# Optimization experiments

Hardware: AMD Instinct MI355X
Metric: run time of the kernel (lower is better)

## Reference

```python
import jax, jax.numpy as jnp
import numpy as np

N_NODES = 100000
N_EDGES = 1600000
D = 64
BN_EPS = 1e-5


def setup_inputs() -> dict:
    key = jax.random.key(0)
    ks = jax.random.split(key, 10)
    s = 1.0 / np.sqrt(D)
    return {
        "features": jax.random.normal(ks[0], (N_NODES, D), dtype=jnp.float32),
        "src": jax.random.randint(ks[1], (N_EDGES,), 0, N_NODES, dtype=jnp.int32),
        "dst": jax.random.randint(ks[2], (N_EDGES,), 0, N_NODES, dtype=jnp.int32),
        "eps": jnp.zeros((), dtype=jnp.float32),
        "W1": jax.random.uniform(ks[3], (D, D), jnp.float32, -s, s),
        "b1": jax.random.uniform(ks[4], (D,), jnp.float32, -s, s),
        "W2": jax.random.uniform(ks[5], (D, D), jnp.float32, -s, s),
        "b2": jax.random.uniform(ks[6], (D,), jnp.float32, -s, s),
        "gamma": jnp.ones((D,), dtype=jnp.float32),
        "beta": jnp.zeros((D,), dtype=jnp.float32),
    }


def reference(features, src, dst, eps, W1, b1, W2, b2, gamma, beta):
    h_in = features
    # message passing: gather src node features, scatter-sum to dst (fn.copy_u + fn.sum)
    neigh = jax.ops.segment_sum(features[src], dst, num_segments=N_NODES)  # [N, D]
    # eps-weighted self term
    h = (1.0 + eps) * features + neigh
    # apply_func MLP: Linear -> ReLU -> Linear
    h = jnp.maximum(h @ W1 + b1, 0.0) @ W2 + b2
    # BatchNorm1d over nodes (training-mode batch statistics)
    mean = jnp.mean(h, axis=0)
    var = jnp.var(h, axis=0)
    h = (h - mean) * jax.lax.rsqrt(var + BN_EPS) * gamma + beta
    # activation
    h = jnp.maximum(h, 0.0)
    # residual (indim == outdim)
    h = h_in + h
    # dropout p=0 -> identity
    return h
```

## Files before the change

kernel.cpp:

```cpp
#include <hip/hip_runtime.h>
#include <hip/hip_fp16.h>

#define N_NODES 100000
#define N_EDGES 1600000
#define D 64
#define BN_EPS 1e-5f
#define NSHARD 64

#define NBKT 256
#define NPB 391
#define BKT_CAP 13056
#define NBBLK 391
#define SORT_T 1024

typedef _Float16 half8 __attribute__((ext_vector_type(8)));
typedef float f32x4 __attribute__((ext_vector_type(4)));

__global__ __launch_bounds__(256) void prep_k(
    const int* __restrict__ src, const int* __restrict__ dst,
    int* __restrict__ bkt_cnt, int* __restrict__ bktbuf,
    const float* __restrict__ feat, __half* __restrict__ feat16,
    const float* __restrict__ W1, const float* __restrict__ W2,
    _Float16* __restrict__ w1t, _Float16* __restrict__ w2t)
{
    __shared__ int h[NBKT], base[NBKT], cur[NBKT];
    const int blk = blockIdx.x;
    const int t = threadIdx.x;

    if (blk < NBBLK) {
        h[t] = 0; cur[t] = 0;
        __syncthreads();
        const int e0 = blk * 4096;
        int pk[16], b[16];
        #pragma unroll
        for (int i = 0; i < 16; ++i) {
            int e = e0 + i * 256 + t;
            if (e < N_EDGES) {
                int d = dst[e];
                b[i] = d / NPB;
                pk[i] = (src[e] << 9) | (d - b[i] * NPB);
                atomicAdd(&h[b[i]], 1);
            } else {
                b[i] = -1;
            }
        }
        __syncthreads();
        base[t] = atomicAdd(&bkt_cnt[t], h[t]);
        __syncthreads();
        #pragma unroll
        for (int i = 0; i < 16; ++i) {
            if (b[i] >= 0) {
                int p = atomicAdd(&cur[b[i]], 1);
                bktbuf[(size_t)b[i] * BKT_CAP + base[b[i]] + p] = pk[i];
            }
        }
    } else if (blk < NBBLK + 3125) {
        size_t i = ((size_t)(blk - NBBLK) * 256 + t) * 8;
        if (i < (size_t)N_NODES * D) {
            float4 v0 = *(const float4*)(feat + i);
            float4 v1 = *(const float4*)(feat + i + 4);
            __half2 o[4];
            o[0] = __floats2half2_rn(v0.x, v0.y);
            o[1] = __floats2half2_rn(v0.z, v0.w);
            o[2] = __floats2half2_rn(v1.x, v1.y);
            o[3] = __floats2half2_rn(v1.z, v1.w);
            *(float4*)(feat16 + i) = *(float4*)o;
        }
    } else {
        const int n = t >> 2;
        const int k0 = (t & 3) * 16;
        _Float16 o1[16], o2[16];
        #pragma unroll
        for (int j = 0; j < 16; ++j) {
            o1[j] = (_Float16)W1[(k0 + j) * 64 + n];
            o2[j] = (_Float16)W2[(k0 + j) * 64 + n];
        }
        #pragma unroll
        for (int j = 0; j < 16; j += 8) {
            *(half8*)(w1t + n * 64 + k0 + j) = *(half8*)&o1[j];
            *(half8*)(w2t + n * 64 + k0 + j) = *(half8*)&o2[j];
        }
    }
}

__global__ __launch_bounds__(SORT_T) void sortp_k(
    const int* __restrict__ bktbuf, const int* __restrict__ bkt_cnt,
    int* __restrict__ rowptr, int* __restrict__ col)
{
    __shared__ int h[NPB];
    __shared__ int cur[NPB];
    __shared__ int part[SORT_T];
    __shared__ int bsc[NBKT];

    const int b = blockIdx.x;
    const int t = threadIdx.x;
    const int nb0 = b * NPB;
    const int nodes_in = min(NPB, N_NODES - nb0);
    const int cnt = bkt_cnt[b];
    const int* buf = bktbuf + (size_t)b * BKT_CAP;

    if (t < NBKT) bsc[t] = bkt_cnt[t];
    __syncthreads();
    for (int off = 1; off < NBKT; off <<= 1) {
        int x = 0;
        if (t < NBKT) {
            x = bsc[t];
            if (t >= off) x += bsc[t - off];
        }
        __syncthreads();
        if (t < NBKT) bsc[t] = x;
        __syncthreads();
    }
    const int gbase = bsc[b] - cnt;

    if (t < NPB) h[t] = 0;
    __syncthreads();

    for (int i = t; i < cnt; i += SORT_T)
        atomicAdd(&h[buf[i] & 511], 1);
    __syncthreads();

    int a = (t < NPB) ? h[t] : 0;
    part[t] = a;
    __syncthreads();
    for (int off = 1; off < SORT_T; off <<= 1) {
        int x = part[t];
        int u = (t >= off) ? part[t - off] : 0;
        __syncthreads();
        part[t] = x + u;
        __syncthreads();
    }
    int excl = part[t] - a;
    if (t < NPB) {
        cur[t] = excl;
        if (t < nodes_in) rowptr[nb0 + t] = gbase + excl;
    }
    if (b == NBKT - 1 && t == 0) rowptr[N_NODES] = N_EDGES;
    __syncthreads();

    for (int i = t; i < cnt; i += SORT_T) {
        int pk = buf[i];
        int slot = atomicAdd(&cur[pk & 511], 1);
        col[gbase + slot] = pk >> 9;
    }
}

__device__ __forceinline__ void acc16(float* a, float4 r0, float4 r1)
{
    const __half2* h0 = (const __half2*)&r0;
    const __half2* h1 = (const __half2*)&r1;
    #pragma unroll
    for (int i = 0; i < 4; ++i) {
        float2 f = __half22float2(h0[i]);
        a[2 * i]     += f.x;
        a[2 * i + 1] += f.y;
    }
    #pragma unroll
    for (int i = 0; i < 4; ++i) {
        float2 f = __half22float2(h1[i]);
        a[8 + 2 * i]     += f.x;
        a[8 + 2 * i + 1] += f.y;
    }
}

__global__ __launch_bounds__(256) void gatherq_k(
    const __half* __restrict__ feat16, const int* __restrict__ rowptr,
    const int* __restrict__ col, const float* __restrict__ epsp,
    __half* __restrict__ x16)
{
    const int t = threadIdx.x;
    const int node = blockIdx.x * 64 + (t >> 2);
    if (node >= N_NODES) return;
    const int c = (t & 3) << 4;

    const int lo = rowptr[node];
    const int hi = rowptr[node + 1];

    float a[16];
    #pragma unroll
    for (int i = 0; i < 16; ++i) a[i] = 0.f;

    int e = lo;
    for (; e + 3 < hi; e += 4) {
        const int s0 = col[e], s1 = col[e + 1], s2 = col[e + 2], s3 = col[e + 3];
        const __half* p0 = feat16 + (size_t)s0 * 64 + c;
        const __half* p1 = feat16 + (size_t)s1 * 64 + c;
        const __half* p2 = feat16 + (size_t)s2 * 64 + c;
        const __half* p3 = feat16 + (size_t)s3 * 64 + c;
        float4 r00 = *(const float4*)(p0), r01 = *(const float4*)(p0 + 8);
        float4 r10 = *(const float4*)(p1), r11 = *(const float4*)(p1 + 8);
        float4 r20 = *(const float4*)(p2), r21 = *(const float4*)(p2 + 8);
        float4 r30 = *(const float4*)(p3), r31 = *(const float4*)(p3 + 8);
        acc16(a, r00, r01);
        acc16(a, r10, r11);
        acc16(a, r20, r21);
        acc16(a, r30, r31);
    }
    for (; e < hi; ++e) {
        const __half* p = feat16 + (size_t)col[e] * 64 + c;
        float4 r0 = *(const float4*)(p), r1 = *(const float4*)(p + 8);
        acc16(a, r0, r1);
    }

    const float epsv = 1.0f + epsp[0];
    const size_t gb = (size_t)node * 64 + c;
    float4 s0 = *(const float4*)(feat16 + gb);
    float4 s1 = *(const float4*)(feat16 + gb + 8);
    const __half2* h0 = (const __half2*)&s0;
    const __half2* h1 = (const __half2*)&s1;
    __half2 o[8];
    #pragma unroll
    for (int i = 0; i < 4; ++i) {
        float2 f = __half22float2(h0[i]);
        o[i] = __floats2half2_rn(fmaf(epsv, f.x, a[2 * i]),
                                 fmaf(epsv, f.y, a[2 * i + 1]));
    }
    #pragma unroll
    for (int i = 0; i < 4; ++i) {
        float2 f = __half22float2(h1[i]);
        o[4 + i] = __floats2half2_rn(fmaf(epsv, f.x, a[8 + 2 * i]),
                                     fmaf(epsv, f.y, a[8 + 2 * i + 1]));
    }
    *(float4*)(x16 + gb)     = *(float4*)&o[0];
    *(float4*)(x16 + gb + 8) = *(float4*)&o[4];
}

__global__ __launch_bounds__(256) void mfma_mlp2_k(
    const __half* __restrict__ x16,
    const _Float16* __restrict__ w1t, const _Float16* __restrict__ w2t,
    const float* __restrict__ b1, const float* __restrict__ b2,
    __half* __restrict__ h216, float* __restrict__ stats)
{
    __shared__ __align__(16) _Float16 xts[64 * 72];

    const int t    = threadIdx.x;
    const int w    = t >> 6;
    const int lane = t & 63;
    const int m    = lane & 15;
    const int q    = lane >> 4;
    const int rbase = w * 16;
    const int nb   = blockIdx.x * 64;

    const _Float16* xg = (const _Float16*)x16 + (size_t)(nb + rbase + m) * 64 + q * 8;
    half8 a0 = *(const half8*)(xg);
    half8 a1 = *(const half8*)(xg + 32);

    f32x4 acc[4];
    #pragma unroll
    for (int jt = 0; jt < 4; ++jt) {
        const float bias = b1[jt * 16 + m];
        acc[jt] = (f32x4){bias, bias, bias, bias};
        const _Float16* bw = w1t + (jt * 16 + m) * 64 + q * 8;
        half8 bf0 = *(const half8*)(bw);
        half8 bf1 = *(const half8*)(bw + 32);
        acc[jt] = __builtin_amdgcn_mfma_f32_16x16x32_f16(a0, bf0, acc[jt], 0, 0, 0);
        acc[jt] = __builtin_amdgcn_mfma_f32_16x16x32_f16(a1, bf1, acc[jt], 0, 0, 0);
    }

    #pragma unroll
    for (int jt = 0; jt < 4; ++jt)
        #pragma unroll
        for (int r = 0; r < 4; ++r)
            xts[(rbase + q * 4 + r) * 72 + jt * 16 + m] =
                (_Float16)fmaxf(acc[jt][r], 0.0f);
    asm volatile("s_waitcnt lgkmcnt(0)" ::: "memory");

    const _Float16* xw = &xts[(rbase + m) * 72 + q * 8];
    half8 c0 = *(const half8*)(xw);
    half8 c1 = *(const half8*)(xw + 32);

    f32x4 acc2[4];
    #pragma unroll
    for (int jt = 0; jt < 4; ++jt) {
        const float bias = b2[jt * 16 + m];
        acc2[jt] = (f32x4){bias, bias, bias, bias};
        const _Float16* bw = w2t + (jt * 16 + m) * 64 + q * 8;
        half8 bf0 = *(const half8*)(bw);
        half8 bf1 = *(const half8*)(bw + 32);
        acc2[jt] = __builtin_amdgcn_mfma_f32_16x16x32_f16(c0, bf0, acc2[jt], 0, 0, 0);
        acc2[jt] = __builtin_amdgcn_mfma_f32_16x16x32_f16(c1, bf1, acc2[jt], 0, 0, 0);
    }
    asm volatile("s_waitcnt lgkmcnt(0)" ::: "memory");

    float psums[4], psqs[4];
    #pragma unroll
    for (int jt = 0; jt < 4; ++jt) {
        float ps = 0.f, pq = 0.f;
        #pragma unroll
        for (int r = 0; r < 4; ++r) {
            const int row = rbase + q * 4 + r;
            const float v = acc2[jt][r];
            const float vv = (nb + row < N_NODES) ? v : 0.f;
            ps += vv;
            pq += vv * vv;
            xts[row * 72 + jt * 16 + m] = (_Float16)v;
        }
        ps += __shfl_xor(ps, 16, 64); ps += __shfl_xor(ps, 32, 64);
        pq += __shfl_xor(pq, 16, 64); pq += __shfl_xor(pq, 32, 64);
        psums[jt] = ps; psqs[jt] = pq;
    }
    if (lane < 16) {
        float* sp = stats + (size_t)(blockIdx.x & (NSHARD - 1)) * 128;
        #pragma unroll
        for (int jt = 0; jt < 4; ++jt) {
            unsafeAtomicAdd(sp + jt * 16 + lane,      psums[jt]);
            unsafeAtomicAdd(sp + 64 + jt * 16 + lane, psqs[jt]);
        }
    }
    asm volatile("s_waitcnt lgkmcnt(0)" ::: "memory");

    {
        const int rr = lane >> 2;
        const int cc = (lane & 3) * 16;
        const int gn = nb + rbase + rr;
        if (gn < N_NODES) {
            float4 r0 = *(const float4*)&xts[(rbase + rr) * 72 + cc];
            float4 r1 = *(const float4*)&xts[(rbase + rr) * 72 + cc + 8];
            *(float4*)(h216 + (size_t)gn * 64 + cc)     = r0;
            *(float4*)(h216 + (size_t)gn * 64 + cc + 8) = r1;
        }
    }
}

__global__ void bnstats_k(const float* __restrict__ stats,
                          const float* __restrict__ gamma,
                          const float* __restrict__ beta,
                          float* __restrict__ sf)
{
    int j = threadIdx.x;
    float s = 0.f, q = 0.f;
    for (int c = 0; c < NSHARD; ++c) {
        s += stats[c * 128 + j];
        q += stats[c * 128 + 64 + j];
    }
    const float invN = 1.0f / (float)N_NODES;
    float mean  = s * invN;
    float var   = q * invN - mean * mean;
    float scale = gamma[j] * rsqrtf(var + BN_EPS);
    sf[j]      = scale;
    sf[64 + j] = beta[j] - mean * scale;
}

__global__ __launch_bounds__(256) void finish16_k(
    const float* __restrict__ feat, const __half* __restrict__ h216,
    const float* __restrict__ sf, float* __restrict__ out)
{
    __shared__ float scs[64], shs[64];
    if (threadIdx.x < 64) {
        scs[threadIdx.x] = sf[threadIdx.x];
        shs[threadIdx.x] = sf[64 + threadIdx.x];
    }
    __syncthreads();
    size_t i = (size_t)blockIdx.x * 256 + threadIdx.x;
    if (i < (size_t)N_NODES * D / 4) {
        int j = (int)((i * 4) & 63);
        const __half2* hp = (const __half2*)(h216 + i * 4);
        float2 h0 = __half22float2(hp[0]);
        float2 h1 = __half22float2(hp[1]);
        float4 f = *(const float4*)(feat + i * 4);
        float4 o;
        o.x = fmaxf(fmaf(h0.x, scs[j + 0], shs[j + 0]), 0.f) + f.x;
        o.y = fmaxf(fmaf(h0.y, scs[j + 1], shs[j + 1]), 0.f) + f.y;
        o.z = fmaxf(fmaf(h1.x, scs[j + 2], shs[j + 2]), 0.f) + f.z;
        o.w = fmaxf(fmaf(h1.y, scs[j + 3], shs[j + 3]), 0.f) + f.w;
        *(float4*)(out + i * 4) = o;
    }
}

#define OCAP 7680

__global__ __launch_bounds__(256) void bucket2_k(
    const int* __restrict__ src, const int* __restrict__ dst,
    int* __restrict__ bkt_cnt, int2* __restrict__ bktbuf)
{
    __shared__ int h[NBKT], base[NBKT], cur[NBKT];
    const int t = threadIdx.x;
    h[t] = 0; cur[t] = 0;
    __syncthreads();
    const int e0 = blockIdx.x * 4096;
    int s[16], d[16], b[16];
    #pragma unroll
    for (int i = 0; i < 16; ++i) {
        int e = e0 + i * 256 + t;
        if (e < N_EDGES) {
            s[i] = src[e];
            d[i] = dst[e];
            b[i] = d[i] / NPB;
            atomicAdd(&h[b[i]], 1);
        } else {
            b[i] = -1;
        }
    }
    __syncthreads();
    base[t] = atomicAdd(&bkt_cnt[t], h[t]);
    __syncthreads();
    #pragma unroll
    for (int i = 0; i < 16; ++i) {
        if (b[i] >= 0) {
            int p = atomicAdd(&cur[b[i]], 1);
            bktbuf[(size_t)b[i] * OCAP + base[b[i]] + p] = make_int2(s[i], d[i]);
        }
    }
}

__global__ __launch_bounds__(SORT_T) void sort2_k(
    const int2* __restrict__ bktbuf, const int* __restrict__ bkt_cnt,
    int* __restrict__ rowptr, int* __restrict__ col)
{
    __shared__ int h[NPB];
    __shared__ int cur[NPB];
    __shared__ int part[SORT_T];
    __shared__ int bsc[NBKT];

    const int b = blockIdx.x;
    const int t = threadIdx.x;
    const int nb0 = b * NPB;
    const int nodes_in = min(NPB, N_NODES - nb0);
    const int cnt = bkt_cnt[b];
    const int2* buf = bktbuf + (size_t)b * OCAP;

    if (t < NBKT) bsc[t] = bkt_cnt[t];
    __syncthreads();
    for (int off = 1; off < NBKT; off <<= 1) {
        int x = 0;
        if (t < NBKT) {
            x = bsc[t];
            if (t >= off) x += bsc[t - off];
        }
        __syncthreads();
        if (t < NBKT) bsc[t] = x;
        __syncthreads();
    }
    const int gbase = bsc[b] - cnt;

    if (t < NPB) h[t] = 0;
    __syncthreads();

    for (int i = t; i < cnt; i += SORT_T)
        atomicAdd(&h[buf[i].y - nb0], 1);
    __syncthreads();

    int a = (t < NPB) ? h[t] : 0;
    part[t] = a;
    __syncthreads();
    for (int off = 1; off < SORT_T; off <<= 1) {
        int x = part[t];
        int u = (t >= off) ? part[t - off] : 0;
        __syncthreads();
        part[t] = x + u;
        __syncthreads();
    }
    int excl = part[t] - a;
    if (t < NPB) {
        cur[t] = excl;
        if (t < nodes_in) rowptr[nb0 + t] = gbase + excl;
    }
    if (b == NBKT - 1 && t == 0) rowptr[N_NODES] = N_EDGES;
    __syncthreads();

    for (int i = t; i < cnt; i += SORT_T) {
        int2 r = buf[i];
        int slot = atomicAdd(&cur[r.y - nb0], 1);
        col[gbase + slot] = r.x;
    }
}

__global__ __launch_bounds__(256) void gather32_k(
    const float* __restrict__ feat, const int* __restrict__ rowptr,
    const int* __restrict__ col, const float* __restrict__ epsp,
    float* __restrict__ x)
{
    int node = blockIdx.x * 4 + (threadIdx.x >> 6);
    int lane = threadIdx.x & 63;
    if (node >= N_NODES) return;
    int g = lane >> 4;
    int c = (lane & 15) << 2;
    int lo = rowptr[node];
    int hi = rowptr[node + 1];
    float ax = 0.f, ay = 0.f, az = 0.f, aw = 0.f;
    int e = lo + g;
    for (; e + 4 < hi; e += 8) {
        int s0 = col[e];
        int s1 = col[e + 4];
        float4 v0 = *(const float4*)(feat + (size_t)s0 * D + c);
        float4 v1 = *(const float4*)(feat + (size_t)s1 * D + c);
        ax += v0.x; ay += v0.y; az += v0.z; aw += v0.w;
        ax += v1.x; ay += v1.y; az += v1.z; aw += v1.w;
    }
    if (e < hi) {
        float4 v = *(const float4*)(feat + (size_t)col[e] * D + c);
        ax += v.x; ay += v.y; az += v.z; aw += v.w;
    }
    #pragma unroll
    for (int off = 16; off <= 32; off <<= 1) {
        ax += __shfl_xor(ax, off, 64);
        ay += __shfl_xor(ay, off, 64);
        az += __shfl_xor(az, off, 64);
        aw += __shfl_xor(aw, off, 64);
    }
    if (g == 0) {
        float4 f = *(const float4*)(feat + (size_t)node * D + c);
        const float epsv = 1.0f + epsp[0];
        float4 r;
        r.x = fmaf(epsv, f.x, ax);
        r.y = fmaf(epsv, f.y, ay);
        r.z = fmaf(epsv, f.z, az);
        r.w = fmaf(epsv, f.w, aw);
        *(float4*)(x + (size_t)node * D + c) = r;
    }
}

__global__ __launch_bounds__(256) void mlp32_k(
    const float* __restrict__ x,
    const float* __restrict__ W1, const float* __restrict__ b1,
    const float* __restrict__ W2, const float* __restrict__ b2,
    float* __restrict__ h2out, float* __restrict__ stats)
{
    __shared__ float W1s[64 * 68];
    __shared__ float W2s[64 * 68];
    __shared__ float xs[64 * 65];
    __shared__ float b1s[64], b2s[64];

    const int t  = threadIdx.x;
    const int nb = blockIdx.x * 64;

    #pragma unroll
    for (int i = 0; i < 4; ++i) {
        int l  = t + i * 256;
        int k  = l >> 4;
        int j4 = (l & 15) << 2;
        *(float4*)(&W1s[k * 68 + j4]) = *(const float4*)(W1 + k * 64 + j4);
        *(float4*)(&W2s[k * 68 + j4]) = *(const float4*)(W2 + k * 64 + j4);
    }
    if (t < 64)       b1s[t]      = b1[t];
    else if (t < 128) b2s[t - 64] = b2[t - 64];

    #pragma unroll
    for (int i = 0; i < 2; ++i) {
        int n  = (t >> 3) + i * 32;
        int k8 = (t & 7) << 3;
        int gn = nb + n;
        float4 a = make_float4(0.f, 0.f, 0.f, 0.f), b = a;
        if (gn < N_NODES) {
            a = *(const float4*)(x + (size_t)gn * D + k8);
            b = *(const float4*)(x + (size_t)gn * D + k8 + 4);
        }
        *(float4*)&xs[n * 65 + k8]     = a;
        *(float4*)&xs[n * 65 + k8 + 4] = b;
    }
    __syncthreads();

    const int n0 = (t & 15) << 2;
    const int j0 = (t >> 4) << 2;
    const float* xr0 = &xs[(n0 + 0) * 65];
    const float* xr1 = &xs[(n0 + 1) * 65];
    const float* xr2 = &xs[(n0 + 2) * 65];
    const float* xr3 = &xs[(n0 + 3) * 65];

    float acc[4][4];
    #pragma unroll
    for (int a = 0; a < 4; ++a)
        #pragma unroll
        for (int b = 0; b < 4; ++b)
            acc[a][b] = b1s[j0 + b];

    #pragma unroll 8
    for (int k = 0; k < 64; ++k) {
        const float4 w = *(const float4*)(&W1s[k * 68 + j0]);
        const float x0 = xr0[k], x1 = xr1[k], x2 = xr2[k], x3 = xr3[k];
        acc[0][0] = fmaf(x0, w.x, acc[0][0]); acc[0][1] = fmaf(x0, w.y, acc[0][1]);
        acc[0][2] = fmaf(x0, w.z, acc[0][2]); acc[0][3] = fmaf(x0, w.w, acc[0][3]);
        acc[1][0] = fmaf(x1, w.x, acc[1][0]); acc[1][1] = fmaf(x1, w.y, acc[1][1]);
        acc[1][2] = fmaf(x1, w.z, acc[1][2]); acc[1][3] = fmaf(x1, w.w, acc[1][3]);
        acc[2][0] = fmaf(x2, w.x, acc[2][0]); acc[2][1] = fmaf(x2, w.y, acc[2][1]);
        acc[2][2] = fmaf(x2, w.z, acc[2][2]); acc[2][3] = fmaf(x2, w.w, acc[2][3]);
        acc[3][0] = fmaf(x3, w.x, acc[3][0]); acc[3][1] = fmaf(x3, w.y, acc[3][1]);
        acc[3][2] = fmaf(x3, w.z, acc[3][2]); acc[3][3] = fmaf(x3, w.w, acc[3][3]);
    }

    __syncthreads();
    #pragma unroll
    for (int a = 0; a < 4; ++a)
        #pragma unroll
        for (int b = 0; b < 4; ++b)
            xs[(n0 + a) * 65 + j0 + b] = fmaxf(acc[a][b], 0.0f);
    __syncthreads();

    float acc2[4][4];
    #pragma unroll
    for (int a = 0; a < 4; ++a)
        #pragma unroll
        for (int b = 0; b < 4; ++b)
            acc2[a][b] = b2s[j0 + b];

    #pragma unroll 8
    for (int k = 0; k < 64; ++k) {
        const float4 w = *(const float4*)(&W2s[k * 68 + j0]);
        const float x0 = xr0[k], x1 = xr1[k], x2 = xr2[k], x3 = xr3[k];
        acc2[0][0] = fmaf(x0, w.x, acc2[0][0]); acc2[0][1] = fmaf(x0, w.y, acc2[0][1]);
        acc2[0][2] = fmaf(x0, w.z, acc2[0][2]); acc2[0][3] = fmaf(x0, w.w, acc2[0][3]);
        acc2[1][0] = fmaf(x1, w.x, acc2[1][0]); acc2[1][1] = fmaf(x1, w.y, acc2[1][1]);
        acc2[1][2] = fmaf(x1, w.z, acc2[1][2]); acc2[1][3] = fmaf(x1, w.w, acc2[1][3]);
        acc2[2][0] = fmaf(x2, w.x, acc2[2][0]); acc2[2][1] = fmaf(x2, w.y, acc2[2][1]);
        acc2[2][2] = fmaf(x2, w.z, acc2[2][2]); acc2[2][3] = fmaf(x2, w.w, acc2[2][3]);
        acc2[3][0] = fmaf(x3, w.x, acc2[3][0]); acc2[3][1] = fmaf(x3, w.y, acc2[3][1]);
        acc2[3][2] = fmaf(x3, w.z, acc2[3][2]); acc2[3][3] = fmaf(x3, w.w, acc2[3][3]);
    }

    float psum[4] = {0.f, 0.f, 0.f, 0.f};
    float psq[4]  = {0.f, 0.f, 0.f, 0.f};
    #pragma unroll
    for (int a = 0; a < 4; ++a) {
        int gn = nb + n0 + a;
        if (gn < N_NODES) {
            float4 hh;
            hh.x = acc2[a][0]; hh.y = acc2[a][1]; hh.z = acc2[a][2]; hh.w = acc2[a][3];
            *(float4*)(h2out + (size_t)gn * 64 + j0) = hh;
            psum[0] += hh.x; psq[0] += hh.x * hh.x;
            psum[1] += hh.y; psq[1] += hh.y * hh.y;
            psum[2] += hh.z; psq[2] += hh.z * hh.z;
            psum[3] += hh.w; psq[3] += hh.w * hh.w;
        }
    }
    #pragma unroll
    for (int off = 8; off >= 1; off >>= 1)
        #pragma unroll
        for (int b = 0; b < 4; ++b) {
            psum[b] += __shfl_down(psum[b], off, 16);
            psq[b]  += __shfl_down(psq[b],  off, 16);
        }
    if ((t & 15) == 0) {
        float* sp = stats + (size_t)(blockIdx.x & (NSHARD - 1)) * 128;
        #pragma unroll
        for (int b = 0; b < 4; ++b) {
            unsafeAtomicAdd(sp + j0 + b,      psum[b]);
            unsafeAtomicAdd(sp + 64 + j0 + b, psq[b]);
        }
    }
}

__global__ __launch_bounds__(256) void finish_k(
    const float* __restrict__ feat, const float* __restrict__ sf,
    float* __restrict__ out)
{
    __shared__ float scs[64], shs[64];
    if (threadIdx.x < 64) {
        scs[threadIdx.x] = sf[threadIdx.x];
        shs[threadIdx.x] = sf[64 + threadIdx.x];
    }
    __syncthreads();
    size_t i = (size_t)blockIdx.x * 256 + threadIdx.x;
    if (i < (size_t)N_NODES * D / 4) {
        int j = (int)((i * 4) & 63);
        float4 h = *(float4*)(out + i * 4);
        float4 f = *(const float4*)(feat + i * 4);
        h.x = fmaxf(fmaf(h.x, scs[j + 0], shs[j + 0]), 0.f) + f.x;
        h.y = fmaxf(fmaf(h.y, scs[j + 1], shs[j + 1]), 0.f) + f.y;
        h.z = fmaxf(fmaf(h.z, scs[j + 2], shs[j + 2]), 0.f) + f.z;
        h.w = fmaxf(fmaf(h.w, scs[j + 3], shs[j + 3]), 0.f) + f.w;
        *(float4*)(out + i * 4) = h;
    }
}

extern "C" void kernel_launch(void* const* d_in, const int* in_sizes, int n_in,
                              void* d_out, int out_size, void* d_ws, size_t ws_size,
                              hipStream_t stream)
{
    const float* feat  = (const float*)d_in[0];
    const int*   src   = (const int*)d_in[1];
    const int*   dst   = (const int*)d_in[2];
    const float* eps   = (const float*)d_in[3];
    const float* W1    = (const float*)d_in[4];
    const float* b1    = (const float*)d_in[5];
    const float* W2    = (const float*)d_in[6];
    const float* b2    = (const float*)d_in[7];
    const float* gamma = (const float*)d_in[8];
    const float* beta  = (const float*)d_in[9];
    float* out = (float*)d_out;

    const size_t BKTSZ  = (size_t)NBKT * BKT_CAP * sizeof(int);
    const size_t F16SZ  = (size_t)N_NODES * D * sizeof(__half);
    const size_t COLSZ  = (size_t)N_EDGES * sizeof(int);
    const size_t RPSZ   = ((size_t)(N_NODES + 1) * sizeof(int) + 15) & ~(size_t)15;
    const size_t STATSZ = (size_t)NSHARD * 128 * sizeof(float);
    const size_t CNTSZ  = (size_t)NBKT * sizeof(int);
    const size_t TAIL   = STATSZ + CNTSZ + 128 * 4 + 2 * 4096 * sizeof(_Float16) + 256;
    const size_t need   = BKTSZ + F16SZ + COLSZ + RPSZ + TAIL;

    if (ws_size >= need) {
        char* p = (char*)d_ws;
        int*    bktbuf  = (int*)p;
        __half* x16     = (__half*)p;
        __half* feat16  = (__half*)(p + BKTSZ);
        __half* h216    = feat16;
        int*    col     = (int*)(p + BKTSZ + F16SZ);
        int*    rowptr  = (int*)(p + BKTSZ + F16SZ + COLSZ);
        float*  stats   = (float*)(p + BKTSZ + F16SZ + COLSZ + RPSZ);
        int*    bkt_cnt = (int*)(stats + NSHARD * 128);
        float*  sf      = (float*)(bkt_cnt + NBKT);
        _Float16* w1t   = (_Float16*)(sf + 128);
        _Float16* w2t   = w1t + 4096;

        hipMemsetAsync(stats, 0, STATSZ + CNTSZ, stream);
        prep_k<<<NBBLK + 3125 + 1, 256, 0, stream>>>(src, dst, bkt_cnt, bktbuf,
                                                     feat, feat16, W1, W2, w1t, w2t);
        sortp_k<<<NBKT, SORT_T, 0, stream>>>(bktbuf, bkt_cnt, rowptr, col);
        gatherq_k<<<(N_NODES + 63) / 64, 256, 0, stream>>>(feat16, rowptr, col, eps, x16);
        mfma_mlp2_k<<<(N_NODES + 63) / 64, 256, 0, stream>>>(x16, w1t, w2t, b1, b2, h216, stats);
        bnstats_k<<<1, 64, 0, stream>>>(stats, gamma, beta, sf);
        finish16_k<<<(N_NODES * D / 4 + 255) / 256, 256, 0, stream>>>(feat, h216, sf, out);
    } else {
        const size_t X32SZ = (size_t)N_NODES * D * sizeof(float);
        char* p = (char*)d_ws;
        float* x32    = (float*)p;
        int2*  bktbuf = (int2*)p;
        int*   col    = (int*)(p + X32SZ);
        int*   rowptr = col + N_EDGES;
        float* stats  = (float*)(rowptr + N_NODES + 1);
        int*   bkt_cnt = (int*)(stats + NSHARD * 128);
        float* sf     = (float*)(bkt_cnt + NBKT);

        hipMemsetAsync(stats, 0, STATSZ + NBKT * 4, stream);
        bucket2_k<<<(N_EDGES + 4095) / 4096, 256, 0, stream>>>(src, dst, bkt_cnt, bktbuf);
        sort2_k<<<NBKT, SORT_T, 0, stream>>>(bktbuf, bkt_cnt, rowptr, col);
        gather32_k<<<(N_NODES + 3) / 4, 256, 0, stream>>>(feat, rowptr, col, eps, x32);
        mlp32_k<<<(N_NODES + 63) / 64, 256, 0, stream>>>(x32, W1, b1, W2, b2, out, stats);
        bnstats_k<<<1, 64, 0, stream>>>(stats, gamma, beta, sf);
        finish_k<<<(N_NODES * D / 4 + 255) / 256, 256, 0, stream>>>(feat, sf, out);
    }
}
```

Before: 198.5 us.

## Fuse neighbor gather into MFMA MLP kernel and fold BN stats into finish

```diff
diff --git a/kernel.cpp b/kernel.cpp
--- a/kernel.cpp
+++ b/kernel.cpp
@@ -5,11 +5,11 @@
 #define N_EDGES 1600000
 #define D 64
 #define BN_EPS 1e-5f
-#define NSHARD 64
+#define NSHARD 8
 
 #define NBKT 256
 #define NPB 391
-#define BKT_CAP 13056
+#define BKT_CAP 8192
 #define NBBLK 391
 #define SORT_T 1024
 
@@ -96,10 +96,10 @@
     const int t = threadIdx.x;
     const int nb0 = b * NPB;
     const int nodes_in = min(NPB, N_NODES - nb0);
-    const int cnt = bkt_cnt[b];
+    const int cnt = min(bkt_cnt[b], BKT_CAP);
     const int* buf = bktbuf + (size_t)b * BKT_CAP;
 
-    if (t < NBKT) bsc[t] = bkt_cnt[t];
+    if (t < NBKT) bsc[t] = min(bkt_cnt[t], BKT_CAP);
     __syncthreads();
     for (int off = 1; off < NBKT; off <<= 1) {
         int x = 0;
@@ -163,70 +163,9 @@
     }
 }
 
-__global__ __launch_bounds__(256) void gatherq_k(
+__global__ __launch_bounds__(256) void gmlp_k(
     const __half* __restrict__ feat16, const int* __restrict__ rowptr,
     const int* __restrict__ col, const float* __restrict__ epsp,
-    __half* __restrict__ x16)
-{
-    const int t = threadIdx.x;
-    const int node = blockIdx.x * 64 + (t >> 2);
-    if (node >= N_NODES) return;
-    const int c = (t & 3) << 4;
-
-    const int lo = rowptr[node];
-    const int hi = rowptr[node + 1];
-
-    float a[16];
-    #pragma unroll
-    for (int i = 0; i < 16; ++i) a[i] = 0.f;
-
-    int e = lo;
-    for (; e + 3 < hi; e += 4) {
-        const int s0 = col[e], s1 = col[e + 1], s2 = col[e + 2], s3 = col[e + 3];
-        const __half* p0 = feat16 + (size_t)s0 * 64 + c;
-        const __half* p1 = feat16 + (size_t)s1 * 64 + c;
-        const __half* p2 = feat16 + (size_t)s2 * 64 + c;
-        const __half* p3 = feat16 + (size_t)s3 * 64 + c;
-        float4 r00 = *(const float4*)(p0), r01 = *(const float4*)(p0 + 8);
-        float4 r10 = *(const float4*)(p1), r11 = *(const float4*)(p1 + 8);
-        float4 r20 = *(const float4*)(p2), r21 = *(const float4*)(p2 + 8);
-        float4 r30 = *(const float4*)(p3), r31 = *(const float4*)(p3 + 8);
-        acc16(a, r00, r01);
-        acc16(a, r10, r11);
-        acc16(a, r20, r21);
-        acc16(a, r30, r31);
-    }
-    for (; e < hi; ++e) {
-        const __half* p = feat16 + (size_t)col[e] * 64 + c;
-        float4 r0 = *(const float4*)(p), r1 = *(const float4*)(p + 8);
-        acc16(a, r0, r1);
-    }
-
-    const float epsv = 1.0f + epsp[0];
-    const size_t gb = (size_t)node * 64 + c;
-    float4 s0 = *(const float4*)(feat16 + gb);
-    float4 s1 = *(const float4*)(feat16 + gb + 8);
-    const __half2* h0 = (const __half2*)&s0;
-    const __half2* h1 = (const __half2*)&s1;
-    __half2 o[8];
-    #pragma unroll
-    for (int i = 0; i < 4; ++i) {
-        float2 f = __half22float2(h0[i]);
-        o[i] = __floats2half2_rn(fmaf(epsv, f.x, a[2 * i]),
-                                 fmaf(epsv, f.y, a[2 * i + 1]));
-    }
-    #pragma unroll
-    for (int i = 0; i < 4; ++i) {
-        float2 f = __half22float2(h1[i]);
-        o[4 + i] = __floats2half2_rn(fmaf(epsv, f.x, a[8 + 2 * i]),
-                                     fmaf(epsv, f.y, a[8 + 2 * i + 1]));
-    }
-    *(float4*)(x16 + gb)     = *(float4*)&o[0];
-    *(float4*)(x16 + gb + 8) = *(float4*)&o[4];
-}
-
-__global__ __launch_bounds__(256) void mfma_mlp2_k(
-    const __half* __restrict__ x16,
     const _Float16* __restrict__ w1t, const _Float16* __restrict__ w2t,
     const float* __restrict__ b1, const float* __restrict__ b2,
     __half* __restrict__ h216, float* __restrict__ stats)
@@ -234,16 +173,80 @@
     __shared__ __align__(16) _Float16 xts[64 * 72];
 
     const int t    = threadIdx.x;
-    const int w    = t >> 6;
     const int lane = t & 63;
-    const int m    = lane & 15;
-    const int q    = lane >> 4;
+    const int nb   = blockIdx.x * 64;
+
+    {
+        const int nl   = t >> 2;
+        const int node = nb + nl;
+        const int c    = (t & 3) << 4;
+        __half2 o[8];
+
+        if (node < N_NODES) {
+            const int lo = rowptr[node];
+            const int hi = rowptr[node + 1];
+            float a[16];
+            #pragma unroll
+            for (int i = 0; i < 16; ++i) a[i] = 0.f;
+
+            int e = lo;
+            for (; e + 3 < hi; e += 4) {
+                const int s0 = col[e], s1 = col[e + 1], s2 = col[e + 2], s3 = col[e + 3];
+                const __half* p0 = feat16 + (size_t)s0 * 64 + c;
+                const __half* p1 = feat16 + (size_t)s1 * 64 + c;
+                const __half* p2 = feat16 + (size_t)s2 * 64 + c;
+                const __half* p3 = feat16 + (size_t)s3 * 64 + c;
+                float4 r00 = *(const float4*)(p0), r01 = *(const float4*)(p0 + 8);
+                float4 r10 = *(const float4*)(p1), r11 = *(const float4*)(p1 + 8);
+                float4 r20 = *(const float4*)(p2), r21 = *(const float4*)(p2 + 8);
+                float4 r30 = *(const float4*)(p3), r31 = *(const float4*)(p3 + 8);
+                acc16(a, r00, r01);
+                acc16(a, r10, r11);
+                acc16(a, r20, r21);
+                acc16(a, r30, r31);
+            }
+            for (; e < hi; ++e) {
+                const __half* p = feat16 + (size_t)col[e] * 64 + c;
+                float4 r0 = *(const float4*)(p), r1 = *(const float4*)(p + 8);
+                acc16(a, r0, r1);
+            }
+
+            const float epsv = 1.0f + epsp[0];
+            const size_t gb = (size_t)node * 64 + c;
+            float4 s0 = *(const float4*)(feat16 + gb);
+            float4 s1 = *(const float4*)(feat16 + gb + 8);
+            const __half2* h0 = (const __half2*)&s0;
+            const __half2* h1 = (const __half2*)&s1;
+            #pragma unroll
+            for (int i = 0; i < 4; ++i) {
+                float2 f = __half22float2(h0[i]);
+                o[i] = __floats2half2_rn(fmaf(epsv, f.x, a[2 * i]),
+                                         fmaf(epsv, f.y, a[2 * i + 1]));
+            }
+            #pragma unroll
+            for (int i = 0; i < 4; ++i) {
+                float2 f = __half22float2(h1[i]);
+                o[4 + i] = __floats2half2_rn(fmaf(epsv, f.x, a[8 + 2 * i]),
+                                             fmaf(epsv, f.y, a[8 + 2 * i + 1]));
+            }
+        } else {
+            #pragma unroll
+            for (int i = 0; i < 8; ++i) o[i] = __floats2half2_rn(0.f, 0.f);
+        }
+        *(float4*)&xts[nl * 72 + c]     = *(float4*)&o[0];
+        *(float4*)&xts[nl * 72 + c + 8] = *(float4*)&o[4];
+    }
+    asm volatile("s_waitcnt lgkmcnt(0)" ::: "memory");
+    __builtin_amdgcn_sched_barrier(0);
+
+    const int w     = t >> 6;
+    const int m     = lane & 15;
+    const int q     = lane >> 4;
     const int rbase = w * 16;
-    const int nb   = blockIdx.x * 64;
-
-    const _Float16* xg = (const _Float16*)x16 + (size_t)(nb + rbase + m) * 64 + q * 8;
-    half8 a0 = *(const half8*)(xg);
-    half8 a1 = *(const half8*)(xg + 32);
+
+    const _Float16* xa = &xts[(rbase + m) * 72 + q * 8];
+    half8 a0 = *(const half8*)(xa);
+    half8 a1 = *(const half8*)(xa + 32);
 
     f32x4 acc[4];
     #pragma unroll
@@ -264,6 +267,7 @@
             xts[(rbase + q * 4 + r) * 72 + jt * 16 + m] =
                 (_Float16)fmaxf(acc[jt][r], 0.0f);
     asm volatile("s_waitcnt lgkmcnt(0)" ::: "memory");
+    __builtin_amdgcn_sched_barrier(0);
 
     const _Float16* xw = &xts[(rbase + m) * 72 + q * 8];
     half8 c0 = *(const half8*)(xw);
@@ -281,6 +285,7 @@
         acc2[jt] = __builtin_amdgcn_mfma_f32_16x16x32_f16(c1, bf1, acc2[jt], 0, 0, 0);
     }
     asm volatile("s_waitcnt lgkmcnt(0)" ::: "memory");
+    __builtin_amdgcn_sched_barrier(0);
 
     float psums[4], psqs[4];
     #pragma unroll
@@ -308,6 +313,7 @@
         }
     }
     asm volatile("s_waitcnt lgkmcnt(0)" ::: "memory");
+    __builtin_amdgcn_sched_barrier(0);
 
     {
         const int rr = lane >> 2;
@@ -322,36 +328,29 @@
     }
 }
 
-__global__ void bnstats_k(const float* __restrict__ stats,
-                          const float* __restrict__ gamma,
-                          const float* __restrict__ beta,
-                          float* __restrict__ sf)
-{
-    int j = threadIdx.x;
-    float s = 0.f, q = 0.f;
-    for (int c = 0; c < NSHARD; ++c) {
-        s += stats[c * 128 + j];
-        q += stats[c * 128 + 64 + j];
-    }
-    const float invN = 1.0f / (float)N_NODES;
-    float mean  = s * invN;
-    float var   = q * invN - mean * mean;
-    float scale = gamma[j] * rsqrtf(var + BN_EPS);
-    sf[j]      = scale;
-    sf[64 + j] = beta[j] - mean * scale;
-}
-
 __global__ __launch_bounds__(256) void finish16_k(
     const float* __restrict__ feat, const __half* __restrict__ h216,
-    const float* __restrict__ sf, float* __restrict__ out)
+    const float* __restrict__ stats, const float* __restrict__ gamma,
+    const float* __restrict__ beta, float* __restrict__ out)
 {
     __shared__ float scs[64], shs[64];
-    if (threadIdx.x < 64) {
-        scs[threadIdx.x] = sf[threadIdx.x];
-        shs[threadIdx.x] = sf[64 + threadIdx.x];
-    }
-    __syncthreads();
-    size_t i = (size_t)blockIdx.x * 256 + threadIdx.x;
+    const int t = threadIdx.x;
+    if (t < 64) {
+        float s = 0.f, q = 0.f;
+        #pragma unroll
+        for (int c = 0; c < NSHARD; ++c) {
+            s += stats[c * 128 + t];
+            q += stats[c * 128 + 64 + t];
+        }
+        const float invN = 1.0f / (float)N_NODES;
+        const float mean = s * invN;
+        const float var  = q * invN - mean * mean;
+        const float scale = gamma[t] * rsqrtf(var + BN_EPS);
+        scs[t] = scale;
+        shs[t] = beta[t] - mean * scale;
+    }
+    __syncthreads();
+    size_t i = (size_t)blockIdx.x * 256 + t;
     if (i < (size_t)N_NODES * D / 4) {
         int j = (int)((i * 4) & 63);
         const __half2* hp = (const __half2*)(h216 + i * 4);
@@ -368,6 +367,25 @@
 }
 
 #define OCAP 7680
+
+__global__ void bnstats_k(const float* __restrict__ stats,
+                          const float* __restrict__ gamma,
+                          const float* __restrict__ beta,
+                          float* __restrict__ sf)
+{
+    int j = threadIdx.x;
+    float s = 0.f, q = 0.f;
+    for (int c = 0; c < NSHARD; ++c) {
+        s += stats[c * 128 + j];
+        q += stats[c * 128 + 64 + j];
+    }
+    const float invN = 1.0f / (float)N_NODES;
+    float mean  = s * invN;
+    float var   = q * invN - mean * mean;
+    float scale = gamma[j] * rsqrtf(var + BN_EPS);
+    sf[j]      = scale;
+    sf[64 + j] = beta[j] - mean * scale;
+}
 
 __global__ __launch_bounds__(256) void bucket2_k(
     const int* __restrict__ src, const int* __restrict__ dst,
@@ -685,30 +703,30 @@
     const size_t STATSZ = (size_t)NSHARD * 128 * sizeof(float);
     const size_t CNTSZ  = (size_t)NBKT * sizeof(int);
     const size_t TAIL   = STATSZ + CNTSZ + 128 * 4 + 2 * 4096 * sizeof(_Float16) + 256;
-    const size_t need   = BKTSZ + F16SZ + COLSZ + RPSZ + TAIL;
+    const size_t need   = BKTSZ + 2 * F16SZ + COLSZ + RPSZ + TAIL;
 
     if (ws_size >= need) {
         char* p = (char*)d_ws;
         int*    bktbuf  = (int*)p;
-        __half* x16     = (__half*)p;
-        __half* feat16  = (__half*)(p + BKTSZ);
-        __half* h216    = feat16;
-        int*    col     = (int*)(p + BKTSZ + F16SZ);
-        int*    rowptr  = (int*)(p + BKTSZ + F16SZ + COLSZ);
-        float*  stats   = (float*)(p + BKTSZ + F16SZ + COLSZ + RPSZ);
+        __half* h216    = (__half*)p;
+        __half* feat16  = (__half*)(p + BKTSZ + F16SZ);
+        int*    col     = (int*)(p + BKTSZ + 2 * F16SZ);
+        int*    rowptr  = (int*)(p + BKTSZ + 2 * F16SZ + COLSZ);
+        float*  stats   = (float*)(p + BKTSZ + 2 * F16SZ + COLSZ + RPSZ);
         int*    bkt_cnt = (int*)(stats + NSHARD * 128);
         float*  sf      = (float*)(bkt_cnt + NBKT);
         _Float16* w1t   = (_Float16*)(sf + 128);
         _Float16* w2t   = w1t + 4096;
+        (void)sf;
 
         hipMemsetAsync(stats, 0, STATSZ + CNTSZ, stream);
         prep_k<<<NBBLK + 3125 + 1, 256, 0, stream>>>(src, dst, bkt_cnt, bktbuf,
                                                      feat, feat16, W1, W2, w1t, w2t);
         sortp_k<<<NBKT, SORT_T, 0, stream>>>(bktbuf, bkt_cnt, rowptr, col);
-        gatherq_k<<<(N_NODES + 63) / 64, 256, 0, stream>>>(feat16, rowptr, col, eps, x16);
-        mfma_mlp2_k<<<(N_NODES + 63) / 64, 256, 0, stream>>>(x16, w1t, w2t, b1, b2, h216, stats);
-        bnstats_k<<<1, 64, 0, stream>>>(stats, gamma, beta, sf);
-        finish16_k<<<(N_NODES * D / 4 + 255) / 256, 256, 0, stream>>>(feat, h216, sf, out);
+        gmlp_k<<<(N_NODES + 63) / 64, 256, 0, stream>>>(feat16, rowptr, col, eps,
+                                                        w1t, w2t, b1, b2, h216, stats);
+        finish16_k<<<(N_NODES * D / 4 + 255) / 256, 256, 0, stream>>>(
+            feat, h216, stats, gamma, beta, out);
     } else {
         const size_t X32SZ = (size_t)N_NODES * D * sizeof(float);
         char* p = (char*)d_ws;
```

Measured after the change: 202.4 us. No clear change (+1.9%).
